# Kernel optimization log

Measured on AMD Instinct MI355X. Metric: run time of the kernel, lower is better.

The kernel has to match this reference:

```python
import jax, jax.numpy as jnp
import numpy as np

B = 2048        # batch
H = 256         # hidden_dim
IN = 320        # input_dim = 256 geo + 64 sem
NOPS = 1883     # num_ops
STEPS = 20      # max_steps


def _gru_cell(x, h, w_ih, w_hh, b_ih, b_hh):
    # PyTorch GRUCell math. gates ordered (r, z, n).
    gi = x @ w_ih.T + b_ih          # (B, 3H)
    gh = h @ w_hh.T + b_hh          # (B, 3H)
    ir, iz, inn = jnp.split(gi, 3, axis=-1)
    hr, hz, hn = jnp.split(gh, 3, axis=-1)
    r = jax.nn.sigmoid(ir + hr)
    z = jax.nn.sigmoid(iz + hz)
    n = jnp.tanh(inn + r * hn)
    return (1.0 - z) * n + z * h


def setup_inputs() -> dict:
    key = jax.random.key(0)
    ks = jax.random.split(key, 18)
    s = 0.05
    f32 = jnp.float32
    return {
        "geo_embed": jax.random.normal(ks[0], (B, 256), dtype=f32),
        "sem_embed": jax.random.normal(ks[1], (B, 64), dtype=f32),
        # GRU layer 0 (input IN -> H)
        "w_ih0": jax.random.normal(ks[2], (3 * H, IN), dtype=f32) * s,
        "w_hh0": jax.random.normal(ks[3], (3 * H, H), dtype=f32) * s,
        "b_ih0": jax.random.normal(ks[4], (3 * H,), dtype=f32) * s,
        "b_hh0": jax.random.normal(ks[5], (3 * H,), dtype=f32) * s,
        # GRU layer 1 (H -> H)
        "w_ih1": jax.random.normal(ks[6], (3 * H, H), dtype=f32) * s,
        "w_hh1": jax.random.normal(ks[7], (3 * H, H), dtype=f32) * s,
        "b_ih1": jax.random.normal(ks[8], (3 * H,), dtype=f32) * s,
        "b_hh1": jax.random.normal(ks[9], (3 * H,), dtype=f32) * s,
        # energy head H -> NOPS
        "w_energy": jax.random.normal(ks[10], (NOPS, H), dtype=f32) * s,
        "b_energy": jax.random.normal(ks[11], (NOPS,), dtype=f32) * s,
        # state_proj (2H -> IN)
        "w_proj": jax.random.normal(ks[12], (IN, 2 * H), dtype=f32) * s,
        "b_proj": jax.random.normal(ks[13], (IN,), dtype=f32) * s,
        # op_proj (256 -> H, no bias)
        "w_op": jax.random.normal(ks[14], (H, 256), dtype=f32) * s,
        # frozen op embedding table (buffer)
        "op_embeds": jax.random.normal(ks[15], (NOPS, 256), dtype=f32),
    }


def reference(geo_embed, sem_embed,
              w_ih0, w_hh0, b_ih0, b_hh0,
              w_ih1, w_hh1, b_ih1, b_hh1,
              w_energy, b_energy, w_proj, b_proj,
              w_op, op_embeds):
    x0 = jnp.concatenate([geo_embed, sem_embed], axis=-1)  # (B, 320)
    h0 = jnp.zeros((geo_embed.shape[0], H), geo_embed.dtype)
    h1 = jnp.zeros_like(h0)
    # project op table once (as in the module)
    opp = op_embeds @ w_op.T                  # (NOPS, H)
    opp_sq = jnp.sum(opp * opp, axis=-1)      # (NOPS,)

    def step(carry, _):
        x, h0, h1 = carry
        h0n = _gru_cell(x, h0, w_ih0, w_hh0, b_ih0, b_hh0)
        h1n = _gru_cell(h0n, h1, w_ih1, w_hh1, b_ih1, b_hh1)
        h_top = h1n                                            # (B, H)
        logits = h_top @ w_energy.T + b_energy                 # (B, NOPS)
        # euclidean cdist via ||a||^2 + ||b||^2 - 2ab (avoids B x NOPS x H)
        d2 = (jnp.sum(h_top * h_top, axis=-1, keepdims=True)
              + opp_sq[None, :]
              - 2.0 * (h_top @ opp.T))
        dists = jnp.sqrt(jnp.maximum(d2, 0.0))
        scores = logits - 0.5 * dists                          # (B, NOPS)
        sel = jnp.argmax(scores, axis=-1)                      # (B,)
        sel_emb = op_embeds[sel]                               # (B, 256)
        x_new = jnp.concatenate([h_top, sel_emb], axis=-1) @ w_proj.T + b_proj
        return (x_new, h0n, h1n), (sel.astype(jnp.int32), scores)

    _, (traj, scores) = jax.lax.scan(step, (x0, h0, h1), None, length=STEPS)
    # traj: (STEPS, B) selected op indices per step; scores: (STEPS, B, NOPS)
    return traj, scores
```

## Files before the change

kernel.cpp:

```cpp
#include <hip/hip_runtime.h>
#include <math.h>

#define B 2048
#define H 256
#define INDIM 320
#define NOPS 1883
#define STEPS 20

typedef _Float16 f16;
typedef _Float16 f16x4 __attribute__((ext_vector_type(4)));
typedef _Float16 f16x8 __attribute__((ext_vector_type(8)));
typedef float f32x4 __attribute__((ext_vector_type(4)));
typedef unsigned long long u64;

#define SWZ(r, s) ((s) ^ ((r) & 3) ^ (((r) >> 2) & 1))

#define GLDS(src, dst) __builtin_amdgcn_global_load_lds( \
    (__attribute__((address_space(1))) void*)(src), \
    (__attribute__((address_space(3))) void*)(dst), 16, 0, 0)

#define S1 (1.0f / 1024.0f)
#define S2 (1.0f / 1048576.0f)

__device__ __forceinline__ void split3(float f, f16& c0, f16& c1, f16& c2) {
    c0 = (f16)f;
    float r1 = f - (float)c0;
    c1 = (f16)(r1 * 1024.0f);
    float r2 = r1 - (float)c1 * S1;
    c2 = (f16)(r2 * 1048576.0f);
}

__global__ __launch_bounds__(256) void init_kernel(const float* __restrict__ geo,
                                                   const float* __restrict__ sem,
                                                   f16* __restrict__ x0, f16* __restrict__ x1,
                                                   f16* __restrict__ x2,
                                                   float* __restrict__ h0f, float* __restrict__ h1f,
                                                   f16* __restrict__ h0c0, f16* __restrict__ h0c1,
                                                   f16* __restrict__ h0c2,
                                                   f16* __restrict__ h1c0, f16* __restrict__ h1c1,
                                                   f16* __restrict__ h1c2,
                                                   float* __restrict__ hsq, u64* __restrict__ amax) {
    int i = blockIdx.x * blockDim.x + threadIdx.x;
    if (i < B * INDIM) {
        int b = i / INDIM, c = i % INDIM;
        float f = (c < 256) ? geo[b * 256 + c] : sem[b * 64 + (c - 256)];
        f16 a, bb, cc;
        split3(f, a, bb, cc);
        x0[i] = a; x1[i] = bb; x2[i] = cc;
    }
    if (i < B * H) {
        h0f[i] = 0.0f; h1f[i] = 0.0f;
        h0c0[i] = (f16)0.0f; h0c1[i] = (f16)0.0f; h0c2[i] = (f16)0.0f;
        h1c0[i] = (f16)0.0f; h1c1[i] = (f16)0.0f; h1c2[i] = (f16)0.0f;
    }
    if (i < B) { hsq[i] = 0.0f; amax[i] = 0ull; }
}

#define BM 64
#define BN 64
#define BK 16
__global__ __launch_bounds__(256) void gemm_tn(const float* __restrict__ A,
                                               const float* __restrict__ Bm,
                                               const float* __restrict__ bias,
                                               float* __restrict__ C,
                                               int M, int N, int K) {
    __shared__ float As[BK][BM];
    __shared__ float Bs[BK][BN];
    int tid = threadIdx.x;
    int bm0 = blockIdx.y * BM;
    int bn0 = blockIdx.x * BN;
    int tx = tid & 15, ty = tid >> 4;
    int lr = tid >> 2;
    int lk = (tid & 3) << 2;

    float acc[4][4];
#pragma unroll
    for (int i = 0; i < 4; ++i)
#pragma unroll
        for (int j = 0; j < 4; ++j) acc[i][j] = 0.0f;

    for (int k0 = 0; k0 < K; k0 += BK) {
        {
            int gr = bm0 + lr;
            float4 v = make_float4(0.f, 0.f, 0.f, 0.f);
            if (gr < M) v = *(const float4*)(A + (size_t)gr * K + k0 + lk);
            As[lk + 0][lr] = v.x; As[lk + 1][lr] = v.y;
            As[lk + 2][lr] = v.z; As[lk + 3][lr] = v.w;
        }
        {
            int gn = bn0 + lr;
            float4 v = make_float4(0.f, 0.f, 0.f, 0.f);
            if (gn < N) v = *(const float4*)(Bm + (size_t)gn * K + k0 + lk);
            Bs[lk + 0][lr] = v.x; Bs[lk + 1][lr] = v.y;
            Bs[lk + 2][lr] = v.z; Bs[lk + 3][lr] = v.w;
        }
        __syncthreads();
#pragma unroll
        for (int k = 0; k < BK; ++k) {
            float a[4], b[4];
#pragma unroll
            for (int i = 0; i < 4; ++i) a[i] = As[k][ty * 4 + i];
#pragma unroll
            for (int j = 0; j < 4; ++j) b[j] = Bs[k][tx * 4 + j];
#pragma unroll
            for (int i = 0; i < 4; ++i)
#pragma unroll
                for (int j = 0; j < 4; ++j) acc[i][j] = fmaf(a[i], b[j], acc[i][j]);
        }
        __syncthreads();
    }
#pragma unroll
    for (int i = 0; i < 4; ++i) {
        int gr = bm0 + ty * 4 + i;
        if (gr >= M) continue;
#pragma unroll
        for (int j = 0; j < 4; ++j) {
            int gc = bn0 + tx * 4 + j;
            if (gc < N) C[(size_t)gr * N + gc] = acc[i][j] + (bias ? bias[gc] : 0.0f);
        }
    }
}

__global__ __launch_bounds__(256) void gemm_nn(const float* __restrict__ A,
                                               const float* __restrict__ Bm,
                                               float* __restrict__ C,
                                               int M, int N, int K) {
    __shared__ float As[BK][BM];
    __shared__ float Bs[BK][BN];
    int tid = threadIdx.x;
    int bm0 = blockIdx.y * BM;
    int bn0 = blockIdx.x * BN;
    int tx = tid & 15, ty = tid >> 4;
    int lr = tid >> 2;
    int lk = (tid & 3) << 2;

    float acc[4][4];
#pragma unroll
    for (int i = 0; i < 4; ++i)
#pragma unroll
        for (int j = 0; j < 4; ++j) acc[i][j] = 0.0f;

    for (int k0 = 0; k0 < K; k0 += BK) {
        {
            int gr = bm0 + lr;
            float4 v = make_float4(0.f, 0.f, 0.f, 0.f);
            if (gr < M) v = *(const float4*)(A + (size_t)gr * K + k0 + lk);
            As[lk + 0][lr] = v.x; As[lk + 1][lr] = v.y;
            As[lk + 2][lr] = v.z; As[lk + 3][lr] = v.w;
        }
        {
            int kk = tid >> 4;
            int n4 = (tid & 15) << 2;
            float4 v = *(const float4*)(Bm + (size_t)(k0 + kk) * N + bn0 + n4);
            Bs[kk][n4 + 0] = v.x; Bs[kk][n4 + 1] = v.y;
            Bs[kk][n4 + 2] = v.z; Bs[kk][n4 + 3] = v.w;
        }
        __syncthreads();
#pragma unroll
        for (int k = 0; k < BK; ++k) {
            float a[4], b[4];
#pragma unroll
            for (int i = 0; i < 4; ++i) a[i] = As[k][ty * 4 + i];
#pragma unroll
            for (int j = 0; j < 4; ++j) b[j] = Bs[k][tx * 4 + j];
#pragma unroll
            for (int i = 0; i < 4; ++i)
#pragma unroll
                for (int j = 0; j < 4; ++j) acc[i][j] = fmaf(a[i], b[j], acc[i][j]);
        }
        __syncthreads();
    }
#pragma unroll
    for (int i = 0; i < 4; ++i) {
        int gr = bm0 + ty * 4 + i;
        if (gr >= M) continue;
#pragma unroll
        for (int j = 0; j < 4; ++j) {
            int gc = bn0 + tx * 4 + j;
            if (gc < N) C[(size_t)gr * N + gc] = acc[i][j];
        }
    }
}

__global__ __launch_bounds__(256) void rowdot_bias(const float* __restrict__ A,
                                                   const float* __restrict__ v,
                                                   const float* __restrict__ b0,
                                                   float* __restrict__ outb) {
    int row = blockIdx.x * 4 + (threadIdx.x >> 6);
    int lane = threadIdx.x & 63;
    if (row >= 768) return;
    float s = 0.0f;
    for (int j = lane; j < 320; j += 64) s = fmaf(A[(size_t)row * 320 + j], v[j], s);
#pragma unroll
    for (int off = 32; off > 0; off >>= 1) s += __shfl_down(s, off);
    if (lane == 0) outb[row] = b0[row] + s;
}

__global__ __launch_bounds__(256) void cvt_rows(const float* __restrict__ A, int rows, int cols,
                                                f16* __restrict__ hi, f16* __restrict__ lo,
                                                float* __restrict__ sq) {
    int row = blockIdx.x * 4 + (threadIdx.x >> 6);
    int lane = threadIdx.x & 63;
    if (row >= rows) return;
    const float* src = A + (size_t)row * cols;
    float s = 0.0f;
    for (int c0 = 0; c0 < cols; c0 += 256) {
        int idx = c0 + lane * 4;
        if (idx < cols) {
            float4 v = *(const float4*)(src + idx);
            float vv[4] = {v.x, v.y, v.z, v.w};
            f16x4 h, l;
#pragma unroll
            for (int j = 0; j < 4; ++j) {
                float f = vv[j];
                f16 hv = (f16)f;
                h[j] = hv;
                l[j] = (f16)((f - (float)hv) * 1024.0f);
                s = fmaf(f, f, s);
            }
            *(f16x4*)(hi + (size_t)row * cols + idx) = h;
            *(f16x4*)(lo + (size_t)row * cols + idx) = l;
        }
    }
    if (sq) {
#pragma unroll
        for (int off = 32; off > 0; off >>= 1) s += __shfl_down(s, off);
        if (lane == 0) sq[row] = s;
    }
}

__global__ __launch_bounds__(256) void cvt3_rows(const float* __restrict__ A, int rows, int cols,
                                                 f16* __restrict__ o0, f16* __restrict__ o1,
                                                 f16* __restrict__ o2) {
    int row = blockIdx.x * 4 + (threadIdx.x >> 6);
    int lane = threadIdx.x & 63;
    if (row >= rows) return;
    const float* src = A + (size_t)row * cols;
    for (int c0 = 0; c0 < cols; c0 += 256) {
        int idx = c0 + lane * 4;
        if (idx < cols) {
            float4 v = *(const float4*)(src + idx);
            float vv[4] = {v.x, v.y, v.z, v.w};
            f16x4 a, b, c;
#pragma unroll
            for (int j = 0; j < 4; ++j) {
                f16 p, q, r;
                split3(vv[j], p, q, r);
                a[j] = p; b[j] = q; c[j] = r;
            }
            *(f16x4*)(o0 + (size_t)row * cols + idx) = a;
            *(f16x4*)(o1 + (size_t)row * cols + idx) = b;
            *(f16x4*)(o2 + (size_t)row * cols + idx) = c;
        }
    }
}

__device__ __forceinline__ void gru_mfma_tile(
    const f16* sA, const f16* sW, int lane, int mfrag, int hhalf,
    f32x4* acc, f32x4* accx, f32x4* accy) {
#pragma unroll
    for (int kslot = 0; kslot < 2; ++kslot) {
        int ar = mfrag * 16 + (lane & 15);
        int asl = SWZ(ar, lane >> 4);
        f16x8 a0 = *(const f16x8*)&sA[kslot * 1024 + ar * 32 + asl * 8];
        f16x8 a1 = *(const f16x8*)&sA[2048 + kslot * 1024 + ar * 32 + asl * 8];
        f16x8 a2 = *(const f16x8*)&sA[4096 + kslot * 1024 + ar * 32 + asl * 8];
#pragma unroll
        for (int g = 0; g < 3; ++g) {
            int br_ = g * 32 + hhalf * 16 + (lane & 15);
            int bsl = SWZ(br_, lane >> 4);
            f16x8 b0 = *(const f16x8*)&sW[kslot * 3072 + br_ * 32 + bsl * 8];
            f16x8 b1 = *(const f16x8*)&sW[6144 + kslot * 3072 + br_ * 32 + bsl * 8];
            f16x8 b2 = *(const f16x8*)&sW[12288 + kslot * 3072 + br_ * 32 + bsl * 8];
            acc[g]  = __builtin_amdgcn_mfma_f32_16x16x32_f16(a0, b0, acc[g], 0, 0, 0);
            accx[g] = __builtin_amdgcn_mfma_f32_16x16x32_f16(a0, b1, accx[g], 0, 0, 0);
            accx[g] = __builtin_amdgcn_mfma_f32_16x16x32_f16(a1, b0, accx[g], 0, 0, 0);
            accy[g] = __builtin_amdgcn_mfma_f32_16x16x32_f16(a0, b2, accy[g], 0, 0, 0);
            accy[g] = __builtin_amdgcn_mfma_f32_16x16x32_f16(a1, b1, accy[g], 0, 0, 0);
            accy[g] = __builtin_amdgcn_mfma_f32_16x16x32_f16(a2, b0, accy[g], 0, 0, 0);
        }
    }
}

__device__ __forceinline__ void gru_phase3(
    const f16* __restrict__ A0, const f16* __restrict__ A1, const f16* __restrict__ A2,
    const f16* __restrict__ W0, const f16* __restrict__ W1, const f16* __restrict__ W2,
    int K, int m0, int c0, int tid, int lane, int mfrag, int hhalf,
    f32x4* acc, f32x4* accx, f32x4* accy, f16* sA, f16* sW) {
    for (int k0 = 0; k0 < K; k0 += 64) {
#pragma unroll
        for (int it = 0; it < 3; ++it) {
            int idx = tid + 256 * it;
            int third = idx >> 8, rem = idx & 255;
            int kslot = rem >> 7, within = rem & 127;
            int row = within >> 2, slot = within & 3;
            const f16* src = (third == 0 ? A0 : third == 1 ? A1 : A2)
                             + (size_t)(m0 + row) * K + k0 + kslot * 32 + SWZ(row, slot) * 8;
            GLDS(src, &sA[idx * 8]);
        }
#pragma unroll
        for (int it = 0; it < 9; ++it) {
            int idx = tid + 256 * it;
            int third = idx / 768;
            int rem = idx - third * 768;
            int kslot = rem / 384;
            int within = rem - kslot * 384;
            int row = within >> 2, slot = within & 3;
            int wr = ((row >> 5) << 8) + c0 + (row & 31);
            const f16* src = (third == 0 ? W0 : third == 1 ? W1 : W2)
                             + (size_t)wr * K + k0 + kslot * 32 + SWZ(row, slot) * 8;
            GLDS(src, &sW[idx * 8]);
        }
        __syncthreads();
        gru_mfma_tile(sA, sW, lane, mfrag, hhalf, acc, accx, accy);
        __syncthreads();
    }
}

__device__ __forceinline__ void gru_phase3_f(
    const f16* __restrict__ H10, const f16* __restrict__ H11, const f16* __restrict__ H12,
    const f16* __restrict__ E0, const f16* __restrict__ E1, const f16* __restrict__ E2,
    const unsigned* __restrict__ sSel,
    const f16* __restrict__ W0, const f16* __restrict__ W1, const f16* __restrict__ W2,
    int m0, int c0, int tid, int lane, int mfrag, int hhalf,
    f32x4* acc, f32x4* accx, f32x4* accy, f16* sA, f16* sW) {
    for (int k0 = 0; k0 < 512; k0 += 64) {
#pragma unroll
        for (int it = 0; it < 3; ++it) {
            int idx = tid + 256 * it;
            int third = idx >> 8, rem = idx & 255;
            int kslot = rem >> 7, within = rem & 127;
            int row = within >> 2, slot = within & 3;
            int keff = k0 + kslot * 32;
            const f16* src;
            if (keff < 256) {
                const f16* base = (third == 0 ? H10 : third == 1 ? H11 : H12);
                src = base + (size_t)(m0 + row) * 256 + keff + SWZ(row, slot) * 8;
            } else {
                const f16* base = (third == 0 ? E0 : third == 1 ? E1 : E2);
                src = base + (size_t)sSel[row] * 256 + (keff - 256) + SWZ(row, slot) * 8;
            }
            GLDS(src, &sA[idx * 8]);
        }
#pragma unroll
        for (int it = 0; it < 9; ++it) {
            int idx = tid + 256 * it;
            int third = idx / 768;
            int rem = idx - third * 768;
            int kslot = rem / 384;
            int within = rem - kslot * 384;
            int row = within >> 2, slot = within & 3;
            int wr = ((row >> 5) << 8) + c0 + (row & 31);
            const f16* src = (third == 0 ? W0 : third == 1 ? W1 : W2)
                             + (size_t)wr * 512 + k0 + kslot * 32 + SWZ(row, slot) * 8;
            GLDS(src, &sW[idx * 8]);
        }
        __syncthreads();
        gru_mfma_tile(sA, sW, lane, mfrag, hhalf, acc, accx, accy);
        __syncthreads();
    }
}

__device__ __forceinline__ void gru_epilogue(
    f32x4* acc, f32x4* accx, f32x4* accy, float gi[3][4],
    const float* bih, const float* bhh,
    const float* Hprevf, float* Hnewf,
    f16* O0, f16* O1, f16* O2, float* hsq_acc,
    int m0, int c0, int lane, int mfrag, int hhalf) {
    int c = c0 + hhalf * 16 + (lane & 15);
    float br = bih[c] + bhh[c];
    float bz = bih[256 + c] + bhh[256 + c];
    float bni = bih[512 + c];
    float bnh = bhh[512 + c];
#pragma unroll
    for (int r = 0; r < 4; ++r) {
        int row = m0 + mfrag * 16 + (lane >> 4) * 4 + r;
        float gh_r = acc[0][r] + accx[0][r] * S1 + accy[0][r] * S2;
        float gh_z = acc[1][r] + accx[1][r] * S1 + accy[1][r] * S2;
        float gh_n = acc[2][r] + accx[2][r] * S1 + accy[2][r] * S2;
        float rg = 1.0f / (1.0f + expf(-(gi[0][r] + gh_r + br)));
        float zg = 1.0f / (1.0f + expf(-(gi[1][r] + gh_z + bz)));
        float ng = tanhf(gi[2][r] + bni + rg * (gh_n + bnh));
        float hp = Hprevf[(size_t)row * 256 + c];
        float o = (1.0f - zg) * ng + zg * hp;
        Hnewf[(size_t)row * 256 + c] = o;
        f16 q0, q1, q2;
        split3(o, q0, q1, q2);
        O0[(size_t)row * 256 + c] = q0;
        O1[(size_t)row * 256 + c] = q1;
        O2[(size_t)row * 256 + c] = q2;
        if (hsq_acc) {
            float sq = o * o;
#pragma unroll
            for (int off = 1; off < 16; off <<= 1) sq += __shfl_xor(sq, off);
            if ((lane & 15) == 0) atomicAdd(hsq_acc + row, sq);
        }
    }
}

__global__ __launch_bounds__(256, 2) void gru_mfma3(
    const f16* __restrict__ A0, const f16* __restrict__ A1, const f16* __restrict__ A2, int K1,
    const f16* __restrict__ Wi0, const f16* __restrict__ Wi1, const f16* __restrict__ Wi2,
    const f16* __restrict__ P0, const f16* __restrict__ P1, const f16* __restrict__ P2,
    const f16* __restrict__ Wh0, const f16* __restrict__ Wh1, const f16* __restrict__ Wh2,
    const float* __restrict__ bih, const float* __restrict__ bhh,
    const float* __restrict__ Hprevf,
    float* __restrict__ Hnewf,
    f16* __restrict__ O0, f16* __restrict__ O1, f16* __restrict__ O2,
    float* __restrict__ hsq_zero, float* __restrict__ hsq_acc,
    u64* __restrict__ amax_zero) {
    __shared__ __align__(16) f16 sA[3 * 2 * 32 * 32];
    __shared__ __align__(16) f16 sW[3 * 2 * 96 * 32];
    int tid = threadIdx.x;
    int lane = tid & 63;
    int wave = tid >> 6;
    int mfrag = wave & 1;
    int hhalf = wave >> 1;
    int c0 = blockIdx.x * 32;
    int m0 = blockIdx.y * 32;

    if (hsq_zero && blockIdx.x == 0 && tid < 32) hsq_zero[m0 + tid] = 0.0f;
    if (amax_zero && blockIdx.x == 0 && tid < 32) amax_zero[m0 + tid] = 0ull;

    f32x4 acc[3], accx[3], accy[3];
#pragma unroll
    for (int g = 0; g < 3; ++g) {
        acc[g] = (f32x4){0.f, 0.f, 0.f, 0.f};
        accx[g] = (f32x4){0.f, 0.f, 0.f, 0.f};
        accy[g] = (f32x4){0.f, 0.f, 0.f, 0.f};
    }

    gru_phase3(A0, A1, A2, Wi0, Wi1, Wi2, K1, m0, c0, tid, lane, mfrag, hhalf,
               acc, accx, accy, sA, sW);

    float gi[3][4];
#pragma unroll
    for (int g = 0; g < 3; ++g)
#pragma unroll
        for (int r = 0; r < 4; ++r) {
            gi[g][r] = acc[g][r] + accx[g][r] * S1 + accy[g][r] * S2;
            acc[g][r] = 0.f; accx[g][r] = 0.f; accy[g][r] = 0.f;
        }

    gru_phase3(P0, P1, P2, Wh0, Wh1, Wh2, 256, m0, c0, tid, lane, mfrag, hhalf,
               acc, accx, accy, sA, sW);

    gru_epilogue(acc, accx, accy, gi, bih, bhh, Hprevf, Hnewf, O0, O1, O2, hsq_acc,
                 m0, c0, lane, mfrag, hhalf);
}

__global__ __launch_bounds__(256, 2) void gru_mfma3_f(
    const f16* __restrict__ H10, const f16* __restrict__ H11, const f16* __restrict__ H12,
    const f16* __restrict__ E0, const f16* __restrict__ E1, const f16* __restrict__ E2,
    const u64* __restrict__ amax,
    const f16* __restrict__ Wc0, const f16* __restrict__ Wc1, const f16* __restrict__ Wc2,
    const f16* __restrict__ P0, const f16* __restrict__ P1, const f16* __restrict__ P2,
    const f16* __restrict__ Wh0, const f16* __restrict__ Wh1, const f16* __restrict__ Wh2,
    const float* __restrict__ bihc, const float* __restrict__ bhh,
    const float* __restrict__ Hprevf,
    float* __restrict__ Hnewf,
    f16* __restrict__ O0, f16* __restrict__ O1, f16* __restrict__ O2,
    float* __restrict__ hsq_zero, float* __restrict__ traj_prev) {
    __shared__ __align__(16) f16 sA[3 * 2 * 32 * 32];
    __shared__ __align__(16) f16 sW[3 * 2 * 96 * 32];
    __shared__ unsigned sSel[32];
    int tid = threadIdx.x;
    int lane = tid & 63;
    int wave = tid >> 6;
    int mfrag = wave & 1;
    int hhalf = wave >> 1;
    int c0 = blockIdx.x * 32;
    int m0 = blockIdx.y * 32;

    if (tid < 32) {
        unsigned selv = 0xFFFFFFFFu - (unsigned)(amax[m0 + tid] & 0xFFFFFFFFull);
        sSel[tid] = selv;
        if (blockIdx.x == 0) {
            traj_prev[m0 + tid] = (float)selv;
            if (hsq_zero) hsq_zero[m0 + tid] = 0.0f;
        }
    }
    __syncthreads();

    f32x4 acc[3], accx[3], accy[3];
#pragma unroll
    for (int g = 0; g < 3; ++g) {
        acc[g] = (f32x4){0.f, 0.f, 0.f, 0.f};
        accx[g] = (f32x4){0.f, 0.f, 0.f, 0.f};
        accy[g] = (f32x4){0.f, 0.f, 0.f, 0.f};
    }

    gru_phase3_f(H10, H11, H12, E0, E1, E2, sSel, Wc0, Wc1, Wc2,
                 m0, c0, tid, lane, mfrag, hhalf, acc, accx, accy, sA, sW);

    float gi[3][4];
#pragma unroll
    for (int g = 0; g < 3; ++g)
#pragma unroll
        for (int r = 0; r < 4; ++r) {
            gi[g][r] = acc[g][r] + accx[g][r] * S1 + accy[g][r] * S2;
            acc[g][r] = 0.f; accx[g][r] = 0.f; accy[g][r] = 0.f;
        }

    gru_phase3(P0, P1, P2, Wh0, Wh1, Wh2, 256, m0, c0, tid, lane, mfrag, hhalf,
               acc, accx, accy, sA, sW);

    gru_epilogue(acc, accx, accy, gi, bihc, bhh, Hprevf, Hnewf, O0, O1, O2, nullptr,
                 m0, c0, lane, mfrag, hhalf);
}

__global__ __launch_bounds__(256, 2) void scores_mfma(
    const f16* __restrict__ Ahh, const f16* __restrict__ All,
    const f16* __restrict__ W1h, const f16* __restrict__ W1l,
    const f16* __restrict__ W2h, const f16* __restrict__ W2l,
    const float* __restrict__ hsq, const float* __restrict__ be,
    const float* __restrict__ osq, float* __restrict__ out,
    u64* __restrict__ amax) {
    __shared__ __align__(16) f16 sA[2 * 2 * 128 * 32];
    __shared__ __align__(16) f16 sB[4 * 2 * 64 * 32];
    int tid = threadIdx.x;
    int lane = tid & 63;
    int wave = tid >> 6;
    int wm = wave >> 1;
    int wn = wave & 1;
    int n0 = blockIdx.x * 64;
    int m0 = blockIdx.y * 128;

    f32x4 acc1[4][2], acc1x[4][2], acc2[4][2], acc2x[4][2];
#pragma unroll
    for (int i = 0; i < 4; ++i)
#pragma unroll
        for (int j = 0; j < 2; ++j) {
            acc1[i][j] = (f32x4){0.f, 0.f, 0.f, 0.f};
            acc1x[i][j] = (f32x4){0.f, 0.f, 0.f, 0.f};
            acc2[i][j] = (f32x4){0.f, 0.f, 0.f, 0.f};
            acc2x[i][j] = (f32x4){0.f, 0.f, 0.f, 0.f};
        }

    for (int k0 = 0; k0 < 256; k0 += 64) {
#pragma unroll
        for (int it = 0; it < 8; ++it) {
            int idx = tid + 256 * it;
            int half = idx >> 10;
            int rem = idx & 1023;
            int kslot = rem >> 9;
            int within = rem & 511;
            int r = within >> 2, slt = within & 3;
            const f16* src = (half ? All : Ahh)
                             + (size_t)(m0 + r) * 256 + k0 + kslot * 32 + SWZ(r, slt) * 8;
            GLDS(src, &sA[idx * 8]);
        }
#pragma unroll
        for (int it = 0; it < 8; ++it) {
            int idx = tid + 256 * it;
            int arr = idx >> 9;
            int rem = idx & 511;
            int kslot = rem >> 8;
            int within = rem & 255;
            int r = within >> 2, slt = within & 3;
            const f16* src = (arr == 0) ? W1h : (arr == 1) ? W1l : (arr == 2) ? W2h : W2l;
            int gn = n0 + r;
            if (gn >= NOPS) gn = 0;
            GLDS(src + (size_t)gn * 256 + k0 + kslot * 32 + SWZ(r, slt) * 8, &sB[idx * 8]);
        }
        __syncthreads();

#pragma unroll
        for (int kslot = 0; kslot < 2; ++kslot) {
            f16x8 ah[4], al[4];
#pragma unroll
            for (int fm = 0; fm < 4; ++fm) {
                int r = wm * 64 + fm * 16 + (lane & 15);
                int sl = SWZ(r, lane >> 4);
                ah[fm] = *(const f16x8*)&sA[kslot * 4096 + r * 32 + sl * 8];
                al[fm] = *(const f16x8*)&sA[8192 + kslot * 4096 + r * 32 + sl * 8];
            }
#pragma unroll
            for (int fn = 0; fn < 2; ++fn) {
                int r = wn * 32 + fn * 16 + (lane & 15);
                int sl = SWZ(r, lane >> 4);
                f16x8 b1h = *(const f16x8*)&sB[kslot * 2048 + r * 32 + sl * 8];
                f16x8 b1l = *(const f16x8*)&sB[4096 + kslot * 2048 + r * 32 + sl * 8];
                f16x8 b2h = *(const f16x8*)&sB[8192 + kslot * 2048 + r * 32 + sl * 8];
                f16x8 b2l = *(const f16x8*)&sB[12288 + kslot * 2048 + r * 32 + sl * 8];
#pragma unroll
                for (int fm = 0; fm < 4; ++fm) {
                    acc1[fm][fn]  = __builtin_amdgcn_mfma_f32_16x16x32_f16(ah[fm], b1h, acc1[fm][fn], 0, 0, 0);
                    acc1x[fm][fn] = __builtin_amdgcn_mfma_f32_16x16x32_f16(al[fm], b1h, acc1x[fm][fn], 0, 0, 0);
                    acc1x[fm][fn] = __builtin_amdgcn_mfma_f32_16x16x32_f16(ah[fm], b1l, acc1x[fm][fn], 0, 0, 0);
                    acc2[fm][fn]  = __builtin_amdgcn_mfma_f32_16x16x32_f16(ah[fm], b2h, acc2[fm][fn], 0, 0, 0);
                    acc2x[fm][fn] = __builtin_amdgcn_mfma_f32_16x16x32_f16(al[fm], b2h, acc2x[fm][fn], 0, 0, 0);
                    acc2x[fm][fn] = __builtin_amdgcn_mfma_f32_16x16x32_f16(ah[fm], b2l, acc2x[fm][fn], 0, 0, 0);
                }
            }
        }
        __syncthreads();
    }

    const float inv = 1.0f / 1024.0f;
    int nn[2]; float bev[2], osv[2]; bool okn[2];
#pragma unroll
    for (int fn = 0; fn < 2; ++fn) {
        nn[fn] = n0 + wn * 32 + fn * 16 + (lane & 15);
        okn[fn] = nn[fn] < NOPS;
        bev[fn] = okn[fn] ? be[nn[fn]] : 0.0f;
        osv[fn] = okn[fn] ? osq[nn[fn]] : 0.0f;
    }
#pragma unroll
    for (int fm = 0; fm < 4; ++fm) {
#pragma unroll
        for (int r = 0; r < 4; ++r) {
            int m = m0 + wm * 64 + fm * 16 + (lane >> 4) * 4 + r;
            float hs = hsq[m];
            u64 bestk = 0ull;
#pragma unroll
            for (int fn = 0; fn < 2; ++fn) {
                if (okn[fn]) {
                    float dot1 = acc1[fm][fn][r] + acc1x[fm][fn][r] * inv;
                    float dot2 = acc2[fm][fn][r] + acc2x[fm][fn][r] * inv;
                    float sc = (dot1 + bev[fn])
                             - 0.5f * sqrtf(fmaxf(hs + osv[fn] - 2.0f * dot2, 0.0f));
                    out[(size_t)m * NOPS + nn[fn]] = sc;
                    unsigned int u = __float_as_uint(sc);
                    unsigned int mono = (u & 0x80000000u) ? ~u : (u | 0x80000000u);
                    u64 key = ((u64)mono << 32) | (u64)(0xFFFFFFFFu - (unsigned)nn[fn]);
                    if (key > bestk) bestk = key;
                }
            }
#pragma unroll
            for (int off = 1; off < 16; off <<= 1) {
                u64 ok = __shfl_xor(bestk, off);
                if (ok > bestk) bestk = ok;
            }
            if ((lane & 15) == 0) atomicMax(amax + m, bestk);
        }
    }
}

__global__ __launch_bounds__(256) void writetraj(const u64* __restrict__ amax,
                                                 float* __restrict__ traj) {
    int i = blockIdx.x * blockDim.x + threadIdx.x;
    if (i < B) {
        unsigned selv = 0xFFFFFFFFu - (unsigned)(amax[i] & 0xFFFFFFFFull);
        traj[i] = (float)selv;
    }
}

extern "C" void kernel_launch(void* const* d_in, const int* in_sizes, int n_in,
                              void* d_out, int out_size, void* d_ws, size_t ws_size,
                              hipStream_t stream) {
    const float* geo      = (const float*)d_in[0];
    const float* sem      = (const float*)d_in[1];
    const float* w_ih0    = (const float*)d_in[2];
    const float* w_hh0    = (const float*)d_in[3];
    const float* b_ih0    = (const float*)d_in[4];
    const float* b_hh0    = (const float*)d_in[5];
    const float* w_ih1    = (const float*)d_in[6];
    const float* w_hh1    = (const float*)d_in[7];
    const float* b_ih1    = (const float*)d_in[8];
    const float* b_hh1    = (const float*)d_in[9];
    const float* w_energy = (const float*)d_in[10];
    const float* b_energy = (const float*)d_in[11];
    const float* w_proj   = (const float*)d_in[12];
    const float* b_proj   = (const float*)d_in[13];
    const float* w_op     = (const float*)d_in[14];
    const float* op_emb   = (const float*)d_in[15];

    char* p = (char*)d_ws;
    auto alloc = [&](size_t bytes) { char* q = p; p += (bytes + 255) & ~255ULL; return q; };
    float* opp   = (float*)alloc((size_t)NOPS * 256 * 4);
    float* oppsq = (float*)alloc((size_t)NOPS * 4);
    float* hsq   = (float*)alloc((size_t)B * 4);
    u64*   amax  = (u64*)  alloc((size_t)B * 8);
    float* wcf   = (float*)alloc((size_t)768 * 512 * 4);
    float* bihc  = (float*)alloc((size_t)768 * 4);
    float *h0f[2], *h1f[2];
    f16 *h0c[2][3], *h1c[2][3];
    for (int i = 0; i < 2; ++i) {
        h0f[i] = (float*)alloc((size_t)B * H * 4);
        h1f[i] = (float*)alloc((size_t)B * H * 4);
        for (int j = 0; j < 3; ++j) {
            h0c[i][j] = (f16*)alloc((size_t)B * H * 2);
            h1c[i][j] = (f16*)alloc((size_t)B * H * 2);
        }
    }
    f16* x0 = (f16*)alloc((size_t)B * INDIM * 2);
    f16* x1 = (f16*)alloc((size_t)B * INDIM * 2);
    f16* x2 = (f16*)alloc((size_t)B * INDIM * 2);
    f16 *wi0[3], *wh0[3], *wi1[3], *wh1[3], *wc[3], *emb[3];
    for (int i = 0; i < 3; ++i) {
        wi0[i] = (f16*)alloc((size_t)768 * 320 * 2);
        wh0[i] = (f16*)alloc((size_t)768 * 256 * 2);
        wi1[i] = (f16*)alloc((size_t)768 * 256 * 2);
        wh1[i] = (f16*)alloc((size_t)768 * 256 * 2);
        wc[i]  = (f16*)alloc((size_t)768 * 512 * 2);
        emb[i] = (f16*)alloc((size_t)NOPS * 256 * 2);
    }
    f16* weh = (f16*)alloc((size_t)NOPS * 256 * 2);
    f16* wel = (f16*)alloc((size_t)NOPS * 256 * 2);
    f16* oph = (f16*)alloc((size_t)NOPS * 256 * 2);
    f16* opl = (f16*)alloc((size_t)NOPS * 256 * 2);

    float* out    = (float*)d_out;
    float* traj   = out;
    float* scores = out + (size_t)STEPS * B;

    init_kernel<<<dim3((B * INDIM + 255) / 256), dim3(256), 0, stream>>>(
        geo, sem, x0, x1, x2, h0f[0], h1f[0],
        h0c[0][0], h0c[0][1], h0c[0][2], h1c[0][0], h1c[0][1], h1c[0][2],
        hsq, amax);
    gemm_tn<<<dim3(256 / BN, (NOPS + BM - 1) / BM), dim3(256), 0, stream>>>(
        op_emb, w_op, nullptr, opp, NOPS, 256, 256);
    gemm_nn<<<dim3(512 / BN, 768 / BM), dim3(256), 0, stream>>>(w_ih0, w_proj, wcf, 768, 512, 320);
    rowdot_bias<<<dim3(192), dim3(256), 0, stream>>>(w_ih0, b_proj, b_ih0, bihc);
    cvt3_rows<<<dim3(192), dim3(256), 0, stream>>>(w_ih0, 768, 320, wi0[0], wi0[1], wi0[2]);
    cvt3_rows<<<dim3(192), dim3(256), 0, stream>>>(w_hh0, 768, 256, wh0[0], wh0[1], wh0[2]);
    cvt3_rows<<<dim3(192), dim3(256), 0, stream>>>(w_ih1, 768, 256, wi1[0], wi1[1], wi1[2]);
    cvt3_rows<<<dim3(192), dim3(256), 0, stream>>>(w_hh1, 768, 256, wh1[0], wh1[1], wh1[2]);
    cvt3_rows<<<dim3(192), dim3(256), 0, stream>>>(wcf, 768, 512, wc[0], wc[1], wc[2]);
    cvt3_rows<<<dim3((NOPS + 3) / 4), dim3(256), 0, stream>>>(op_emb, NOPS, 256, emb[0], emb[1], emb[2]);
    cvt_rows<<<dim3((NOPS + 3) / 4), dim3(256), 0, stream>>>(w_energy, NOPS, 256, weh, wel, nullptr);
    cvt_rows<<<dim3((NOPS + 3) / 4), dim3(256), 0, stream>>>(opp, NOPS, 256, oph, opl, oppsq);

    for (int t = 0; t < STEPS; ++t) {
        int pi = t & 1, po = pi ^ 1;

        if (t == 0) {
            gru_mfma3<<<dim3(H / 32, B / 32), dim3(256), 0, stream>>>(
                x0, x1, x2, INDIM, wi0[0], wi0[1], wi0[2],
                h0c[pi][0], h0c[pi][1], h0c[pi][2], wh0[0], wh0[1], wh0[2],
                b_ih0, b_hh0, h0f[pi], h0f[po], h0c[po][0], h0c[po][1], h0c[po][2],
                hsq, nullptr, nullptr);
        } else {
            gru_mfma3_f<<<dim3(H / 32, B / 32), dim3(256), 0, stream>>>(
                h1c[pi][0], h1c[pi][1], h1c[pi][2],
                emb[0], emb[1], emb[2], amax,
                wc[0], wc[1], wc[2],
                h0c[pi][0], h0c[pi][1], h0c[pi][2], wh0[0], wh0[1], wh0[2],
                bihc, b_hh0, h0f[pi], h0f[po], h0c[po][0], h0c[po][1], h0c[po][2],
                hsq, traj + (size_t)(t - 1) * B);
        }
        gru_mfma3<<<dim3(H / 32, B / 32), dim3(256), 0, stream>>>(
            h0c[po][0], h0c[po][1], h0c[po][2], 256, wi1[0], wi1[1], wi1[2],
            h1c[pi][0], h1c[pi][1], h1c[pi][2], wh1[0], wh1[1], wh1[2],
            b_ih1, b_hh1, h1f[pi], h1f[po], h1c[po][0], h1c[po][1], h1c[po][2],
            nullptr, hsq, amax);

        scores_mfma<<<dim3((NOPS + 63) / 64, B / 128), dim3(256), 0, stream>>>(
            h1c[po][0], h1c[po][1], weh, wel, oph, opl, hsq, b_energy, oppsq,
            scores + (size_t)t * B * NOPS, amax);
    }
    writetraj<<<dim3((B + 255) / 256), dim3(256), 0, stream>>>(amax, traj + (size_t)(STEPS - 1) * B);
}
```

Before: 1.832 ms.

## Merge weight conversion launches into one kernel and swizzle scores block order

```diff
diff --git a/kernel.cpp b/kernel.cpp
--- a/kernel.cpp
+++ b/kernel.cpp
@@ -196,10 +196,10 @@
     if (lane == 0) outb[row] = b0[row] + s;
 }
 
-__global__ __launch_bounds__(256) void cvt_rows(const float* __restrict__ A, int rows, int cols,
-                                                f16* __restrict__ hi, f16* __restrict__ lo,
-                                                float* __restrict__ sq) {
-    int row = blockIdx.x * 4 + (threadIdx.x >> 6);
+__device__ __forceinline__ void cvt2_dev(const float* __restrict__ A, int rows, int cols,
+                                         f16* __restrict__ hi, f16* __restrict__ lo,
+                                         float* __restrict__ sq, int blk) {
+    int row = blk * 4 + (threadIdx.x >> 6);
     int lane = threadIdx.x & 63;
     if (row >= rows) return;
     const float* src = A + (size_t)row * cols;
@@ -229,10 +229,10 @@
     }
 }
 
-__global__ __launch_bounds__(256) void cvt3_rows(const float* __restrict__ A, int rows, int cols,
-                                                 f16* __restrict__ o0, f16* __restrict__ o1,
-                                                 f16* __restrict__ o2) {
-    int row = blockIdx.x * 4 + (threadIdx.x >> 6);
+__device__ __forceinline__ void cvt3_dev(const float* __restrict__ A, int rows, int cols,
+                                         f16* __restrict__ o0, f16* __restrict__ o1,
+                                         f16* __restrict__ o2, int blk) {
+    int row = blk * 4 + (threadIdx.x >> 6);
     int lane = threadIdx.x & 63;
     if (row >= rows) return;
     const float* src = A + (size_t)row * cols;
@@ -253,6 +253,26 @@
             *(f16x4*)(o2 + (size_t)row * cols + idx) = c;
         }
     }
+}
+
+__global__ __launch_bounds__(256) void cvt_all(
+    const float* __restrict__ wih0, f16* a0, f16* a1, f16* a2,
+    const float* __restrict__ whh0, f16* b0, f16* b1, f16* b2,
+    const float* __restrict__ wih1, f16* c0, f16* c1, f16* c2,
+    const float* __restrict__ whh1, f16* d0, f16* d1, f16* d2,
+    const float* __restrict__ wcf,  f16* e0, f16* e1, f16* e2,
+    const float* __restrict__ opemb, f16* f0, f16* f1, f16* f2,
+    const float* __restrict__ wen,  f16* g0, f16* g1,
+    const float* __restrict__ opp,  f16* h0, f16* h1, float* osq) {
+    int b = blockIdx.x;
+    if (b < 192)        cvt3_dev(wih0, 768, 320, a0, a1, a2, b);
+    else if (b < 384)   cvt3_dev(whh0, 768, 256, b0, b1, b2, b - 192);
+    else if (b < 576)   cvt3_dev(wih1, 768, 256, c0, c1, c2, b - 384);
+    else if (b < 768)   cvt3_dev(whh1, 768, 256, d0, d1, d2, b - 576);
+    else if (b < 960)   cvt3_dev(wcf, 768, 512, e0, e1, e2, b - 768);
+    else if (b < 1431)  cvt3_dev(opemb, NOPS, 256, f0, f1, f2, b - 960);
+    else if (b < 1902)  cvt2_dev(wen, NOPS, 256, g0, g1, nullptr, b - 1431);
+    else                cvt2_dev(opp, NOPS, 256, h0, h1, osq, b - 1902);
 }
 
 __device__ __forceinline__ void gru_mfma_tile(
@@ -523,8 +543,10 @@
     int wave = tid >> 6;
     int wm = wave >> 1;
     int wn = wave & 1;
-    int n0 = blockIdx.x * 64;
-    int m0 = blockIdx.y * 128;
+    int flat = blockIdx.y * 30 + blockIdx.x;
+    int swz = (flat & 7) * 60 + (flat >> 3);
+    int n0 = (swz % 30) * 64;
+    int m0 = (swz / 30) * 128;
 
     f32x4 acc1[4][2], acc1x[4][2], acc2[4][2], acc2x[4][2];
 #pragma unroll
@@ -713,14 +735,15 @@
         op_emb, w_op, nullptr, opp, NOPS, 256, 256);
     gemm_nn<<<dim3(512 / BN, 768 / BM), dim3(256), 0, stream>>>(w_ih0, w_proj, wcf, 768, 512, 320);
     rowdot_bias<<<dim3(192), dim3(256), 0, stream>>>(w_ih0, b_proj, b_ih0, bihc);
-    cvt3_rows<<<dim3(192), dim3(256), 0, stream>>>(w_ih0, 768, 320, wi0[0], wi0[1], wi0[2]);
-    cvt3_rows<<<dim3(192), dim3(256), 0, stream>>>(w_hh0, 768, 256, wh0[0], wh0[1], wh0[2]);
-    cvt3_rows<<<dim3(192), dim3(256), 0, stream>>>(w_ih1, 768, 256, wi1[0], wi1[1], wi1[2]);
-    cvt3_rows<<<dim3(192), dim3(256), 0, stream>>>(w_hh1, 768, 256, wh1[0], wh1[1], wh1[2]);
-    cvt3_rows<<<dim3(192), dim3(256), 0, stream>>>(wcf, 768, 512, wc[0], wc[1], wc[2]);
-    cvt3_rows<<<dim3((NOPS + 3) / 4), dim3(256), 0, stream>>>(op_emb, NOPS, 256, emb[0], emb[1], emb[2]);
-    cvt_rows<<<dim3((NOPS + 3) / 4), dim3(256), 0, stream>>>(w_energy, NOPS, 256, weh, wel, nullptr);
-    cvt_rows<<<dim3((NOPS + 3) / 4), dim3(256), 0, stream>>>(opp, NOPS, 256, oph, opl, oppsq);
+    cvt_all<<<dim3(2373), dim3(256), 0, stream>>>(
+        w_ih0, wi0[0], wi0[1], wi0[2],
+        w_hh0, wh0[0], wh0[1], wh0[2],
+        w_ih1, wi1[0], wi1[1], wi1[2],
+        w_hh1, wh1[0], wh1[1], wh1[2],
+        wcf,   wc[0],  wc[1],  wc[2],
+        op_emb, emb[0], emb[1], emb[2],
+        w_energy, weh, wel,
+        opp, oph, opl, oppsq);
 
     for (int t = 0; t < STEPS; ++t) {
         int pi = t & 1, po = pi ^ 1;
```

New measurement: 1.805 ms. No clear change (-1.5%).
